# Optimization experiments

Measured on AMD Instinct MI355X. Metric: run time of the kernel, lower is better.

## Reference

```python
import jax, jax.numpy as jnp
import numpy as np

NUM_HEAD = 8


def setup_inputs() -> dict:
    key = jax.random.key(0)
    k1, k2, k3, k4 = jax.random.split(key, 4)
    B, C, H, W = 16, 512, 64, 64
    x = jax.random.normal(k1, (B, C, H, W), dtype=jnp.float32)
    w_qkv = jax.random.normal(k2, (3 * C, C), dtype=jnp.float32) * 0.02  # Conv2d 1x1, no bias
    w_proj = jax.random.normal(k3, (C, C), dtype=jnp.float32) * 0.02
    b_proj = jax.random.normal(k4, (C,), dtype=jnp.float32) * 0.02
    return {"x": x, "w_qkv": w_qkv, "w_proj": w_proj, "b_proj": b_proj}


def reference(x, w_qkv, w_proj, b_proj):
    B, C, H, W = x.shape
    nh = NUM_HEAD
    hd = C // nh
    scale = hd ** (-0.5)
    # 1x1 conv == channel matmul
    qkv = jnp.einsum('oc,bchw->bohw', w_qkv, x)  # [B, 3C, H, W]
    q, k, v = jnp.split(qkv, 3, axis=1)
    q = q.reshape(B, nh, hd, H * W)
    k = k.reshape(B, nh, hd, H * W)
    v = v.reshape(B, nh, hd, H * W)
    # NOTE: faithful to source: contracts over the spatial (last) axis,
    # producing a [B, nh, hd, hd] matrix.
    attn = jnp.einsum('bnqd,bnkd->bnqk', q, k) * scale
    attn = jax.nn.softmax(attn, axis=-1)
    # Faithful to source: 'k' and 'v' are both summed independently (outer sum),
    # exactly as torch.einsum computes it.
    out = jnp.einsum('bnqk,bnvd->bnqd', attn, v)
    out = out.reshape(B, C, H, W)
    return jnp.einsum('oc,bchw->bohw', w_proj, out) + b_proj[None, :, None, None]
```

## Files before the change

kernel.cpp:

```cpp
#include <hip/hip_runtime.h>

#define CDIM 512
#define NH 8
#define HWDIM 4096
#define TILE 256

__global__ __launch_bounds__(256) void prep_kernel(
    const float* __restrict__ wqkv, const float* __restrict__ wproj,
    float* __restrict__ wvT, float* __restrict__ wp) {
  int idx = blockIdx.x * 256 + threadIdx.x;
  if (idx < 4096) {
    int c = idx >> 3, n = idx & 7;
    const float* p = wqkv + (size_t)(1024 + n * 64) * CDIM + c;
    float s = 0.f;
#pragma unroll 8
    for (int j = 0; j < 64; ++j) s += p[(size_t)j * CDIM];
    wvT[idx] = s;
  } else if (idx < 8192) {
    int i2 = idx - 4096;
    int o = i2 >> 3, n = i2 & 7;
    const float* p = wproj + (size_t)o * CDIM + n * 64;
    float s = 0.f;
#pragma unroll 8
    for (int j = 0; j < 64; ++j) s += p[j];
    wp[i2] = s;
  }
}

__global__ __launch_bounds__(256) void fused_kernel(
    const float* __restrict__ x, const float* __restrict__ bias,
    const float* __restrict__ wvT, const float* __restrict__ wp,
    float* __restrict__ y) {
  __shared__ __align__(16) float sWv[4096];
  __shared__ __align__(16) float sWp[4096];
  __shared__ __align__(16) float sB[512];
  __shared__ __align__(16) float sS[4][NH][TILE];

  const int t = threadIdx.x;
  for (int i = t; i < 4096; i += 256) { sWv[i] = wvT[i]; sWp[i] = wp[i]; }
  for (int i = t; i < 512; i += 256) sB[i] = bias[i];
  __syncthreads();

  const int wave = t >> 6;
  const int lane = t & 63;
  const int pos0 = blockIdx.x * TILE;
  const int b = pos0 >> 12;
  const int hw0 = pos0 & (HWDIM - 1);
  const float* xb = x + ((size_t)b * CDIM) * HWDIM + hw0 + lane * 4;

  float acc[NH][4];
#pragma unroll
  for (int n = 0; n < NH; ++n) {
    acc[n][0] = 0.f; acc[n][1] = 0.f; acc[n][2] = 0.f; acc[n][3] = 0.f;
  }

  const int c0 = wave * 128;
#pragma unroll 8
  for (int cc = 0; cc < 128; ++cc) {
    const int c = c0 + cc;
    const float4 xv = *(const float4*)(xb + (size_t)c * HWDIM);
    const float4 w0 = *(const float4*)&sWv[c * 8];
    const float4 w1 = *(const float4*)&sWv[c * 8 + 4];
    const float wn[8] = {w0.x, w0.y, w0.z, w0.w, w1.x, w1.y, w1.z, w1.w};
    const float xv4[4] = {xv.x, xv.y, xv.z, xv.w};
#pragma unroll
    for (int n = 0; n < NH; ++n) {
#pragma unroll
      for (int p = 0; p < 4; ++p) acc[n][p] = fmaf(wn[n], xv4[p], acc[n][p]);
    }
  }

#pragma unroll
  for (int n = 0; n < NH; ++n) {
    *(float4*)&sS[wave][n][lane * 4] =
        make_float4(acc[n][0], acc[n][1], acc[n][2], acc[n][3]);
  }
  __syncthreads();

  float S4[NH][4];
#pragma unroll
  for (int n = 0; n < NH; ++n) {
    const float4 a0 = *(const float4*)&sS[0][n][lane * 4];
    const float4 a1 = *(const float4*)&sS[1][n][lane * 4];
    const float4 a2 = *(const float4*)&sS[2][n][lane * 4];
    const float4 a3 = *(const float4*)&sS[3][n][lane * 4];
    S4[n][0] = a0.x + a1.x + a2.x + a3.x;
    S4[n][1] = a0.y + a1.y + a2.y + a3.y;
    S4[n][2] = a0.z + a1.z + a2.z + a3.z;
    S4[n][3] = a0.w + a1.w + a2.w + a3.w;
  }

  float* yb = y + ((size_t)b * CDIM) * HWDIM + hw0 + lane * 4;
  const int o0 = wave * 128;
#pragma unroll 4
  for (int oo = 0; oo < 128; ++oo) {
    const int o = o0 + oo;
    const float4 w0 = *(const float4*)&sWp[o * 8];
    const float4 w1 = *(const float4*)&sWp[o * 8 + 4];
    const float wn[8] = {w0.x, w0.y, w0.z, w0.w, w1.x, w1.y, w1.z, w1.w};
    const float bb = sB[o];
    float r[4] = {bb, bb, bb, bb};
#pragma unroll
    for (int n = 0; n < NH; ++n) {
#pragma unroll
      for (int p = 0; p < 4; ++p) r[p] = fmaf(wn[n], S4[n][p], r[p]);
    }
    *(float4*)(yb + (size_t)o * HWDIM) = make_float4(r[0], r[1], r[2], r[3]);
  }
}

extern "C" void kernel_launch(void* const* d_in, const int* in_sizes, int n_in,
                              void* d_out, int out_size, void* d_ws, size_t ws_size,
                              hipStream_t stream) {
  const float* x     = (const float*)d_in[0];
  const float* wqkv  = (const float*)d_in[1];
  const float* wproj = (const float*)d_in[2];
  const float* bproj = (const float*)d_in[3];
  float* y = (float*)d_out;

  float* wvT = (float*)d_ws;
  float* wp  = wvT + 4096;

  prep_kernel<<<32, 256, 0, stream>>>(wqkv, wproj, wvT, wp);
  fused_kernel<<<256, 256, 0, stream>>>(x, bproj, wvT, wp, y);
}
```

Baseline: 270.0 us.

## Split fused kernel into separate reduce and project kernels with more blocks

Replaces the single fused kernel, which ran 256 blocks of 256 positions, with two kernels that each launch 1024 blocks over 64 positions. The first kernel reduces x against the per-head summed V weights, combining channel groups with cross-lane shuffles and shared memory, and writes a small per-head intermediate S to workspace. The second kernel reads S and writes the projected output. Weights are now read from global/L1 instead of being staged in LDS. This is meant to raise parallelism and occupancy on a memory-bound workload, at the cost of an extra launch and a small round-trip of S through global memory.

```diff
diff --git a/kernel.cpp b/kernel.cpp
--- a/kernel.cpp
+++ b/kernel.cpp
@@ -3,109 +3,135 @@
 #define CDIM 512
 #define NH 8
 #define HWDIM 4096
-#define TILE 256
+#define BATCH 16
 
 __global__ __launch_bounds__(256) void prep_kernel(
     const float* __restrict__ wqkv, const float* __restrict__ wproj,
     float* __restrict__ wvT, float* __restrict__ wp) {
   int idx = blockIdx.x * 256 + threadIdx.x;
   if (idx < 4096) {
-    int c = idx >> 3, n = idx & 7;
+    int n = idx >> 9, c = idx & 511;
     const float* p = wqkv + (size_t)(1024 + n * 64) * CDIM + c;
     float s = 0.f;
 #pragma unroll 8
     for (int j = 0; j < 64; ++j) s += p[(size_t)j * CDIM];
-    wvT[idx] = s;
+    wvT[c * 8 + n] = s;
   } else if (idx < 8192) {
     int i2 = idx - 4096;
-    int o = i2 >> 3, n = i2 & 7;
+    int n = i2 >> 9, o = i2 & 511;
     const float* p = wproj + (size_t)o * CDIM + n * 64;
     float s = 0.f;
-#pragma unroll 8
-    for (int j = 0; j < 64; ++j) s += p[j];
-    wp[i2] = s;
+#pragma unroll 4
+    for (int j = 0; j < 16; ++j) {
+      float4 v = *(const float4*)(p + j * 4);
+      s += v.x + v.y + v.z + v.w;
+    }
+    wp[o * 8 + n] = s;
   }
 }
 
-__global__ __launch_bounds__(256) void fused_kernel(
-    const float* __restrict__ x, const float* __restrict__ bias,
-    const float* __restrict__ wvT, const float* __restrict__ wp,
-    float* __restrict__ y) {
-  __shared__ __align__(16) float sWv[4096];
-  __shared__ __align__(16) float sWp[4096];
-  __shared__ __align__(16) float sB[512];
-  __shared__ __align__(16) float sS[4][NH][TILE];
+__global__ __launch_bounds__(256) void s_kernel(
+    const float* __restrict__ x, const float* __restrict__ wvT,
+    float* __restrict__ S) {
+  __shared__ __align__(16) float sPart[4][NH][64];
 
   const int t = threadIdx.x;
-  for (int i = t; i < 4096; i += 256) { sWv[i] = wvT[i]; sWp[i] = wp[i]; }
-  for (int i = t; i < 512; i += 256) sB[i] = bias[i];
-  __syncthreads();
-
   const int wave = t >> 6;
   const int lane = t & 63;
-  const int pos0 = blockIdx.x * TILE;
+  const int f = lane & 15;
+  const int sub = lane >> 4;
+  const int cg = wave * 4 + sub;
+
+  const int pos0 = blockIdx.x * 64;
   const int b = pos0 >> 12;
   const int hw0 = pos0 & (HWDIM - 1);
-  const float* xb = x + ((size_t)b * CDIM) * HWDIM + hw0 + lane * 4;
+
+  const float* xb = x + ((size_t)b * CDIM + (size_t)cg * 32) * HWDIM + hw0 + f * 4;
+  const float* wb = wvT + cg * 32 * 8;
 
   float acc[NH][4];
 #pragma unroll
-  for (int n = 0; n < NH; ++n) {
-    acc[n][0] = 0.f; acc[n][1] = 0.f; acc[n][2] = 0.f; acc[n][3] = 0.f;
-  }
+  for (int n = 0; n < NH; ++n)
+    acc[n][0] = acc[n][1] = acc[n][2] = acc[n][3] = 0.f;
 
-  const int c0 = wave * 128;
 #pragma unroll 8
-  for (int cc = 0; cc < 128; ++cc) {
-    const int c = c0 + cc;
-    const float4 xv = *(const float4*)(xb + (size_t)c * HWDIM);
-    const float4 w0 = *(const float4*)&sWv[c * 8];
-    const float4 w1 = *(const float4*)&sWv[c * 8 + 4];
+  for (int cc = 0; cc < 32; ++cc) {
+    const float4 xv = *(const float4*)(xb + (size_t)cc * HWDIM);
+    const float4 w0 = *(const float4*)(wb + cc * 8);
+    const float4 w1 = *(const float4*)(wb + cc * 8 + 4);
     const float wn[8] = {w0.x, w0.y, w0.z, w0.w, w1.x, w1.y, w1.z, w1.w};
     const float xv4[4] = {xv.x, xv.y, xv.z, xv.w};
 #pragma unroll
-    for (int n = 0; n < NH; ++n) {
+    for (int n = 0; n < NH; ++n)
 #pragma unroll
       for (int p = 0; p < 4; ++p) acc[n][p] = fmaf(wn[n], xv4[p], acc[n][p]);
-    }
   }
 
 #pragma unroll
-  for (int n = 0; n < NH; ++n) {
-    *(float4*)&sS[wave][n][lane * 4] =
-        make_float4(acc[n][0], acc[n][1], acc[n][2], acc[n][3]);
+  for (int n = 0; n < NH; ++n)
+#pragma unroll
+    for (int p = 0; p < 4; ++p) {
+      float v = acc[n][p];
+      v += __shfl_xor(v, 16, 64);
+      v += __shfl_xor(v, 32, 64);
+      acc[n][p] = v;
+    }
+
+  if (sub == 0) {
+#pragma unroll
+    for (int n = 0; n < NH; ++n)
+      *(float4*)&sPart[wave][n][f * 4] =
+          make_float4(acc[n][0], acc[n][1], acc[n][2], acc[n][3]);
   }
   __syncthreads();
 
-  float S4[NH][4];
 #pragma unroll
-  for (int n = 0; n < NH; ++n) {
-    const float4 a0 = *(const float4*)&sS[0][n][lane * 4];
-    const float4 a1 = *(const float4*)&sS[1][n][lane * 4];
-    const float4 a2 = *(const float4*)&sS[2][n][lane * 4];
-    const float4 a3 = *(const float4*)&sS[3][n][lane * 4];
-    S4[n][0] = a0.x + a1.x + a2.x + a3.x;
-    S4[n][1] = a0.y + a1.y + a2.y + a3.y;
-    S4[n][2] = a0.z + a1.z + a2.z + a3.z;
-    S4[n][3] = a0.w + a1.w + a2.w + a3.w;
+  for (int r = 0; r < 2; ++r) {
+    const int v = t + r * 256;
+    const int n = v >> 6, sp = v & 63;
+    const float s =
+        sPart[0][n][sp] + sPart[1][n][sp] + sPart[2][n][sp] + sPart[3][n][sp];
+    S[(size_t)b * NH * HWDIM + (size_t)n * HWDIM + hw0 + sp] = s;
   }
+}
 
-  float* yb = y + ((size_t)b * CDIM) * HWDIM + hw0 + lane * 4;
-  const int o0 = wave * 128;
+__global__ __launch_bounds__(256) void y_kernel(
+    const float* __restrict__ S, const float* __restrict__ wp,
+    const float* __restrict__ bias, float* __restrict__ y) {
+  const int t = threadIdx.x;
+  const int wave = t >> 6;
+  const int lane = t & 63;
+  const int f = lane & 15;
+  const int og = wave * 4 + (lane >> 4);
+
+  const int pos0 = blockIdx.x * 64;
+  const int b = pos0 >> 12;
+  const int hw0 = pos0 & (HWDIM - 1);
+
+  float4 Sv[NH];
+#pragma unroll
+  for (int n = 0; n < NH; ++n)
+    Sv[n] = *(const float4*)(S + (size_t)b * NH * HWDIM + (size_t)n * HWDIM + hw0 + f * 4);
+
+  float* yb = y + ((size_t)b * CDIM + (size_t)og * 32) * HWDIM + hw0 + f * 4;
+  const float* wb = wp + og * 32 * 8;
+  const float* bb = bias + og * 32;
+
 #pragma unroll 4
-  for (int oo = 0; oo < 128; ++oo) {
-    const int o = o0 + oo;
-    const float4 w0 = *(const float4*)&sWp[o * 8];
-    const float4 w1 = *(const float4*)&sWp[o * 8 + 4];
+  for (int i = 0; i < 32; ++i) {
+    const float4 w0 = *(const float4*)(wb + i * 8);
+    const float4 w1 = *(const float4*)(wb + i * 8 + 4);
     const float wn[8] = {w0.x, w0.y, w0.z, w0.w, w1.x, w1.y, w1.z, w1.w};
-    const float bb = sB[o];
-    float r[4] = {bb, bb, bb, bb};
+    const float b0 = bb[i];
+    float r[4] = {b0, b0, b0, b0};
 #pragma unroll
     for (int n = 0; n < NH; ++n) {
-#pragma unroll
-      for (int p = 0; p < 4; ++p) r[p] = fmaf(wn[n], S4[n][p], r[p]);
+      r[0] = fmaf(wn[n], Sv[n].x, r[0]);
+      r[1] = fmaf(wn[n], Sv[n].y, r[1]);
+      r[2] = fmaf(wn[n], Sv[n].z, r[2]);
+      r[3] = fmaf(wn[n], Sv[n].w, r[3]);
     }
-    *(float4*)(yb + (size_t)o * HWDIM) = make_float4(r[0], r[1], r[2], r[3]);
+    *(float4*)(yb + (size_t)i * HWDIM) = make_float4(r[0], r[1], r[2], r[3]);
   }
 }
 
@@ -120,7 +146,9 @@
 
   float* wvT = (float*)d_ws;
   float* wp  = wvT + 4096;
+  float* S   = wp + 4096;
 
   prep_kernel<<<32, 256, 0, stream>>>(wqkv, wproj, wvT, wp);
-  fused_kernel<<<256, 256, 0, stream>>>(x, bproj, wvT, wp, y);
+  s_kernel<<<1024, 256, 0, stream>>>(x, wvT, S);
+  y_kernel<<<1024, 256, 0, stream>>>(S, wp, bproj, y);
 }
```

Measured after the change: 281.0 us. +4.0%, slower.
